# Kernel tuning notes

Measured on AMD Instinct MI355X. Metric: run time of the kernel, lower is better.

The kernel has to match this reference:

```python
import jax, jax.numpy as jnp
import numpy as np

N = 210          # sequence length (== module max_length cap)
DM = 2048        # input feature dim (major and minor)
DK = 1024        # key/query dim
DV = 1024        # value dim
K_CLIP = 32      # relative-position clipping distance


def _make_table(n, k):
    # table[i, j] = clip(j - i, -k, k) + k  (Shaw-style relative position index)
    rel = np.arange(n)[None, :] - np.arange(n)[:, None]
    return jnp.asarray(np.clip(rel, -k, k) + k, dtype=jnp.int32)


def setup_inputs() -> dict:
    key = jax.random.key(0)
    ks = jax.random.split(key, 7)
    X_major = jax.random.normal(ks[0], (N, DM), dtype=jnp.float32)
    X_minor = jax.random.normal(ks[1], (N, DM), dtype=jnp.float32)
    # Linear weights stored as [in, out] for x @ W
    s = 0.02
    Wq = jax.random.normal(ks[2], (DM, DK), dtype=jnp.float32) * s
    Wk = jax.random.normal(ks[3], (DM, DK), dtype=jnp.float32) * s
    Wv = jax.random.normal(ks[4], (DM, DV), dtype=jnp.float32) * s
    Wo = jax.random.normal(ks[5], (DV, DV), dtype=jnp.float32) * s
    wk = jax.random.normal(ks[6], (2 * K_CLIP + 1, DK), dtype=jnp.float32) * s
    table = _make_table(N, K_CLIP)
    return {"X_major": X_major, "X_minor": X_minor, "Wq": Wq, "Wk": Wk,
            "Wv": Wv, "Wo": Wo, "wk": wk, "table": table}


def reference(X_major, X_minor, Wq, Wk, Wv, Wo, wk, table):
    n = X_major.shape[0]
    scale = 1.0 / jnp.sqrt(jnp.asarray(Wq.shape[1], X_major.dtype))
    Q = X_major @ Wq                     # [n, dk]
    K = X_minor @ Wk                     # [n, dk]
    V = X_minor @ Wv                     # [n, dv]
    Qs = Q * scale
    S = Qs @ K.T                         # [n, n] content scores
    Rk = wk[table[:n, :n]]               # [n, n, dk] gathered rel-pos reps
    Sr = jnp.einsum('id,ijd->ij', Qs, Rk)  # [n, n] relative scores
    A = jax.nn.softmax(S + Sr, axis=-1)  # [n, n]
    Y = (A @ V) @ Wo                     # [n, dv]
    return (Y, A)
```

## Files before the change

kernel.cpp:

```cpp
#include <hip/hip_runtime.h>

typedef short bf16x8 __attribute__((ext_vector_type(8)));
typedef float f32x4 __attribute__((ext_vector_type(4)));

#define MFMA16(a, b, c) __builtin_amdgcn_mfma_f32_16x16x32_bf16(a, b, c, 0, 0, 0)

__device__ inline short f2bf(float f) {
  unsigned u = __builtin_bit_cast(unsigned, f);
  u += 0x7FFFu + ((u >> 16) & 1u);
  return (short)(u >> 16);
}
__device__ inline unsigned pack2(float lo, float hi) {
  unsigned a = __builtin_bit_cast(unsigned, lo) + 0x8000u;
  unsigned b = __builtin_bit_cast(unsigned, hi) + 0x8000u;
  return __builtin_amdgcn_perm(b, a, 0x07060302u);
}

__device__ inline void async_cp16(const void* g, void* l) {
  __builtin_amdgcn_global_load_lds(
      (const __attribute__((address_space(1))) unsigned int*)g,
      (__attribute__((address_space(3))) unsigned int*)l, 16, 0, 0);
}

#define SWZ(r, c) ((((r) << 4) + ((c) ^ ((r) & 7))) << 3)


__global__ __launch_bounds__(256) void k_prep(const float* __restrict__ xmaj,
                                              const float* __restrict__ xmin,
                                              const float* __restrict__ wkin,
                                              const float* __restrict__ Wq,
                                              const float* __restrict__ Wk,
                                              const float* __restrict__ Wv,
                                              const float* __restrict__ Wo,
                                              short* __restrict__ xmaj_bf,
                                              short* __restrict__ xmin_bf,
                                              short* __restrict__ kwb,
                                              short* __restrict__ wqt,
                                              short* __restrict__ wkt,
                                              short* __restrict__ wvt,
                                              short* __restrict__ wot) {
  __shared__ short tile[64][72];
  int b = blockIdx.x, t = threadIdx.x;
  if (b < 512) {
    int idx = b * 256 + t;
    if (idx < 107520) {
      float4 v = ((const float4*)xmaj)[idx];
      ((uint2*)xmaj_bf)[idx] = make_uint2(pack2(v.x, v.y), pack2(v.z, v.w));
      float4 u = ((const float4*)xmin)[idx];
      ((uint2*)xmin_bf)[idx] = make_uint2(pack2(u.x, u.y), pack2(u.z, u.w));
    }
    if (idx < 16640) {
      float4 v = ((const float4*)wkin)[idx];
      ((uint2*)(kwb + 210 * 1024))[idx] = make_uint2(pack2(v.x, v.y), pack2(v.z, v.w));
    }
    if (idx < 1664) ((uint4*)(kwb + 275 * 1024))[idx] = make_uint4(0, 0, 0, 0);
    return;
  }
  const float* W;
  short* Wt;
  int kt, nt, dstK;
  if (b < 2048) {
    int wi = (b - 512) >> 9, tl = (b - 512) & 511;
    W = wi == 0 ? Wq : (wi == 1 ? Wk : Wv);
    Wt = wi == 0 ? wqt : (wi == 1 ? wkt : wvt);
    kt = tl >> 4; nt = tl & 15; dstK = 2048;
  } else {
    int tl = b - 2048;
    W = Wo; Wt = wot; kt = tl >> 4; nt = tl & 15; dstK = 1024;
  }
  int k0 = kt * 64, n0 = nt * 64;
  int kp = t >> 4, nl4 = (t & 15) * 4;
  for (int h = 0; h < 2; ++h) {
    int kpp = kp + h * 16;
    const float* g = W + (size_t)(k0 + 2 * kpp) * 1024 + n0 + nl4;
    float4 u = *(const float4*)g;
    float4 v = *(const float4*)(g + 1024);
    *(unsigned*)&tile[nl4 + 0][2 * kpp] = pack2(u.x, v.x);
    *(unsigned*)&tile[nl4 + 1][2 * kpp] = pack2(u.y, v.y);
    *(unsigned*)&tile[nl4 + 2][2 * kpp] = pack2(u.z, v.z);
    *(unsigned*)&tile[nl4 + 3][2 * kpp] = pack2(u.w, v.w);
  }
  __syncthreads();
  int nl = t >> 2, cq = t & 3;
  for (int h = 0; h < 2; ++h) {
    int c = cq + h * 4;
    *(uint4*)(Wt + (size_t)(n0 + nl) * dstK + k0 + c * 8) = *(const uint4*)&tile[nl][c * 8];
  }
}

__global__ __launch_bounds__(256, 1) void k_qkv(const short* __restrict__ xmaj,
                                                const short* __restrict__ xmin,
                                                const short* __restrict__ wqt,
                                                const short* __restrict__ wkt,
                                                const short* __restrict__ wvt,
                                                short* __restrict__ qs,
                                                short* __restrict__ kwb,
                                                short* __restrict__ vt) {
  __shared__ short As[64 * 128];
  __shared__ short Bs[64 * 128];
  int b = blockIdx.x, t = threadIdx.x;
  int x = b & 7, s = b >> 3;
  int ntile = x * 6 + (s >> 2), mtile = s & 3;
  int nn0 = ntile * 64;
  int mat = nn0 >> 10, ncol0 = nn0 & 1023, m0 = mtile * 64;
  const short* A = (mat == 0) ? xmaj : xmin;
  const short* Bt = (mat == 0) ? wqt : (mat == 1 ? wkt : wvt);
  int lane = t & 63, w = t >> 6;
  int wm = w >> 1, wn = w & 1;
  int l15 = lane & 15, l4 = lane >> 4;
  f32x4 acc[2][2] = {};

  for (int k0 = 0; k0 < 2048; k0 += 128) {
    __syncthreads();
#pragma unroll
    for (int j = 0; j < 4; ++j) {
      int sj = t + j * 256;
      int r = sj >> 4, cg = (sj & 15) ^ (r & 7);
      async_cp16(A + (size_t)(m0 + r) * 2048 + k0 + cg * 8, &As[(w * 64 + j * 256) * 8]);
    }
#pragma unroll
    for (int j = 0; j < 4; ++j) {
      int sj = t + j * 256;
      int r = sj >> 4, cg = (sj & 15) ^ (r & 7);
      async_cp16(Bt + (size_t)(ncol0 + r) * 2048 + k0 + cg * 8, &Bs[(w * 64 + j * 256) * 8]);
    }
    __syncthreads();
#pragma unroll
    for (int kk = 0; kk < 4; ++kk) {
      int c = kk * 4 + l4;
      int ra0 = wm * 32 + l15, ra1 = ra0 + 16;
      int rb0 = wn * 32 + l15, rb1 = rb0 + 16;
      bf16x8 a0 = *(const bf16x8*)&As[SWZ(ra0, c)];
      bf16x8 a1 = *(const bf16x8*)&As[SWZ(ra1, c)];
      bf16x8 b0 = *(const bf16x8*)&Bs[SWZ(rb0, c)];
      bf16x8 b1 = *(const bf16x8*)&Bs[SWZ(rb1, c)];
      acc[0][0] = MFMA16(a0, b0, acc[0][0]);
      acc[0][1] = MFMA16(a0, b1, acc[0][1]);
      acc[1][0] = MFMA16(a1, b0, acc[1][0]);
      acc[1][1] = MFMA16(a1, b1, acc[1][1]);
    }
  }

  if (mat < 2) {
    float scale = (mat == 0) ? 0.03125f : 1.0f;
    short* dst = (mat == 0) ? qs : kwb;
#pragma unroll
    for (int mi = 0; mi < 2; ++mi)
#pragma unroll
      for (int ni = 0; ni < 2; ++ni) {
        int r0 = m0 + wm * 32 + mi * 16 + l4 * 4;
        int c = ncol0 + wn * 32 + ni * 16 + l15;
        for (int j = 0; j < 4; ++j) {
          int r = r0 + j;
          if (r < 210) dst[r * 1024 + c] = f2bf(acc[mi][ni][j] * scale);
        }
      }
  } else {
    __syncthreads();
#pragma unroll
    for (int mi = 0; mi < 2; ++mi)
#pragma unroll
      for (int ni = 0; ni < 2; ++ni) {
        int nl = wn * 32 + ni * 16 + l15;
        int ml0 = wm * 32 + mi * 16 + l4 * 4;
        for (int j = 0; j < 4; ++j) As[nl * 72 + ml0 + j] = f2bf(acc[mi][ni][j]);
      }
    __syncthreads();
    for (int h = 0; h < 2; ++h) {
      int idx = t + h * 256;
      int nl = idx >> 3, c8 = idx & 7;
      int mg0 = m0 + c8 * 8;
      short* dstp = vt + (ncol0 + nl) * 256 + mg0;
      if (mg0 + 8 <= 210) {
        *(uint4*)dstp = *(const uint4*)&As[nl * 72 + c8 * 8];
      } else {
        for (int e = 0; e < 8; ++e)
          if (mg0 + e < 210) dstp[e] = As[nl * 72 + c8 * 8 + e];
      }
    }
  }
}

__global__ __launch_bounds__(256, 1) void k_sprime(const short* __restrict__ qs,
                                                   const short* __restrict__ kwb,
                                                   float* __restrict__ Sp) {
  __shared__ short As[32 * 128];
  __shared__ short Bs[64 * 128];
  int n0 = blockIdx.x * 64, m0 = blockIdx.y * 32;
  int t = threadIdx.x, lane = t & 63, w = t >> 6;
  int l15 = lane & 15, l4 = lane >> 4;
  f32x4 acc[2] = {};

  for (int k0 = 0; k0 < 1024; k0 += 128) {
    __syncthreads();
#pragma unroll
    for (int j = 0; j < 2; ++j) {
      int sj = t + j * 256;
      int r = sj >> 4, cg = (sj & 15) ^ (r & 7);
      async_cp16(qs + (size_t)(m0 + r) * 1024 + k0 + cg * 8, &As[(w * 64 + j * 256) * 8]);
    }
#pragma unroll
    for (int j = 0; j < 4; ++j) {
      int sj = t + j * 256;
      int r = sj >> 4, cg = (sj & 15) ^ (r & 7);
      async_cp16(kwb + (size_t)(n0 + r) * 1024 + k0 + cg * 8, &Bs[(w * 64 + j * 256) * 8]);
    }
    __syncthreads();
#pragma unroll
    for (int kk = 0; kk < 4; ++kk) {
      int c = kk * 4 + l4;
      int rb = w * 16 + l15;
      bf16x8 a0 = *(const bf16x8*)&As[SWZ(l15, c)];
      bf16x8 a1 = *(const bf16x8*)&As[SWZ(16 + l15, c)];
      bf16x8 bb = *(const bf16x8*)&Bs[SWZ(rb, c)];
      acc[0] = MFMA16(a0, bb, acc[0]);
      acc[1] = MFMA16(a1, bb, acc[1]);
    }
  }
#pragma unroll
  for (int mi = 0; mi < 2; ++mi) {
    int r0 = m0 + mi * 16 + l4 * 4;
    int col = n0 + w * 16 + l15;
    for (int j = 0; j < 4; ++j) Sp[(r0 + j) * 320 + col] = acc[mi][j];
  }
}

__global__ __launch_bounds__(256) void k_softmax(const float* __restrict__ Sp,
                                                 const int* __restrict__ table,
                                                 short* __restrict__ Abf,
                                                 float* __restrict__ outA) {
  int i = blockIdx.x, t = threadIdx.x;
  if (i >= 210) {
    Abf[i * 256 + t] = 0;
    return;
  }
  __shared__ float srow[288];
  __shared__ float red[4];
  for (int j = t; j < 288; j += 256) srow[j] = Sp[i * 320 + j];
  __syncthreads();
  float logit = -1e30f;
  if (t < 210) {
    int tb = table[i * 210 + t];
    logit = srow[t] + srow[210 + tb];
  }
  float m = logit;
  for (int o = 32; o; o >>= 1) m = fmaxf(m, __shfl_xor(m, o));
  if ((t & 63) == 0) red[t >> 6] = m;
  __syncthreads();
  m = fmaxf(fmaxf(red[0], red[1]), fmaxf(red[2], red[3]));
  float e = (t < 210) ? __expf(logit - m) : 0.0f;
  float s = e;
  for (int o = 32; o; o >>= 1) s += __shfl_xor(s, o);
  __syncthreads();
  if ((t & 63) == 0) red[t >> 6] = s;
  __syncthreads();
  s = red[0] + red[1] + red[2] + red[3];
  float a = e / s;
  Abf[i * 256 + t] = (t < 210) ? f2bf(a) : (short)0;
  if (t < 210) outA[i * 210 + t] = a;
}

__global__ __launch_bounds__(256, 1) void k_av(const short* __restrict__ Abf,
                                               const short* __restrict__ vt,
                                               short* __restrict__ av) {
  __shared__ short As[64 * 128];
  __shared__ short Bs[64 * 128];
  int n0 = blockIdx.x * 64, m0 = blockIdx.y * 64;
  int t = threadIdx.x, lane = t & 63, w = t >> 6;
  int wm = w >> 1, wn = w & 1;
  int l15 = lane & 15, l4 = lane >> 4;
  f32x4 acc[2][2] = {};

  for (int k0 = 0; k0 < 256; k0 += 128) {
    __syncthreads();
#pragma unroll
    for (int j = 0; j < 4; ++j) {
      int sj = t + j * 256;
      int r = sj >> 4, cg = (sj & 15) ^ (r & 7);
      async_cp16(Abf + (size_t)(m0 + r) * 256 + k0 + cg * 8, &As[(w * 64 + j * 256) * 8]);
      async_cp16(vt + (size_t)(n0 + r) * 256 + k0 + cg * 8, &Bs[(w * 64 + j * 256) * 8]);
    }
    __syncthreads();
#pragma unroll
    for (int kk = 0; kk < 4; ++kk) {
      int c = kk * 4 + l4;
      int ra0 = wm * 32 + l15, ra1 = ra0 + 16;
      int rb0 = wn * 32 + l15, rb1 = rb0 + 16;
      bf16x8 a0 = *(const bf16x8*)&As[SWZ(ra0, c)];
      bf16x8 a1 = *(const bf16x8*)&As[SWZ(ra1, c)];
      bf16x8 b0 = *(const bf16x8*)&Bs[SWZ(rb0, c)];
      bf16x8 b1 = *(const bf16x8*)&Bs[SWZ(rb1, c)];
      acc[0][0] = MFMA16(a0, b0, acc[0][0]);
      acc[0][1] = MFMA16(a0, b1, acc[0][1]);
      acc[1][0] = MFMA16(a1, b0, acc[1][0]);
      acc[1][1] = MFMA16(a1, b1, acc[1][1]);
    }
  }
#pragma unroll
  for (int mi = 0; mi < 2; ++mi)
#pragma unroll
    for (int ni = 0; ni < 2; ++ni) {
      int r0 = m0 + wm * 32 + mi * 16 + l4 * 4;
      int c = n0 + wn * 32 + ni * 16 + l15;
      for (int j = 0; j < 4; ++j) {
        int r = r0 + j;
        if (r < 210) av[r * 1024 + c] = f2bf(acc[mi][ni][j]);
      }
    }
}

__global__ __launch_bounds__(256, 1) void k_y(const short* __restrict__ av,
                                              const short* __restrict__ wot,
                                              float* __restrict__ outY) {
  __shared__ short As[64 * 128];
  __shared__ short Bs[64 * 128];
  int n0 = blockIdx.x * 64, m0 = blockIdx.y * 64;
  int t = threadIdx.x, lane = t & 63, w = t >> 6;
  int wm = w >> 1, wn = w & 1;
  int l15 = lane & 15, l4 = lane >> 4;
  f32x4 acc[2][2] = {};

  for (int k0 = 0; k0 < 1024; k0 += 128) {
    __syncthreads();
#pragma unroll
    for (int j = 0; j < 4; ++j) {
      int sj = t + j * 256;
      int r = sj >> 4, cg = (sj & 15) ^ (r & 7);
      async_cp16(av + (size_t)(m0 + r) * 1024 + k0 + cg * 8, &As[(w * 64 + j * 256) * 8]);
      async_cp16(wot + (size_t)(n0 + r) * 1024 + k0 + cg * 8, &Bs[(w * 64 + j * 256) * 8]);
    }
    __syncthreads();
#pragma unroll
    for (int kk = 0; kk < 4; ++kk) {
      int c = kk * 4 + l4;
      int ra0 = wm * 32 + l15, ra1 = ra0 + 16;
      int rb0 = wn * 32 + l15, rb1 = rb0 + 16;
      bf16x8 a0 = *(const bf16x8*)&As[SWZ(ra0, c)];
      bf16x8 a1 = *(const bf16x8*)&As[SWZ(ra1, c)];
      bf16x8 b0 = *(const bf16x8*)&Bs[SWZ(rb0, c)];
      bf16x8 b1 = *(const bf16x8*)&Bs[SWZ(rb1, c)];
      acc[0][0] = MFMA16(a0, b0, acc[0][0]);
      acc[0][1] = MFMA16(a0, b1, acc[0][1]);
      acc[1][0] = MFMA16(a1, b0, acc[1][0]);
      acc[1][1] = MFMA16(a1, b1, acc[1][1]);
    }
  }
#pragma unroll
  for (int mi = 0; mi < 2; ++mi)
#pragma unroll
    for (int ni = 0; ni < 2; ++ni) {
      int r0 = m0 + wm * 32 + mi * 16 + l4 * 4;
      int c = n0 + wn * 32 + ni * 16 + l15;
      for (int j = 0; j < 4; ++j) {
        int r = r0 + j;
        if (r < 210) outY[r * 1024 + c] = acc[mi][ni][j];
      }
    }
}

extern "C" void kernel_launch(void* const* d_in, const int* in_sizes, int n_in,
                              void* d_out, int out_size, void* d_ws, size_t ws_size,
                              hipStream_t stream) {
  const float* Xmaj = (const float*)d_in[0];
  const float* Xmin = (const float*)d_in[1];
  const float* Wq = (const float*)d_in[2];
  const float* Wk = (const float*)d_in[3];
  const float* Wv = (const float*)d_in[4];
  const float* Wo = (const float*)d_in[5];
  const float* wk = (const float*)d_in[6];
  const int* table = (const int*)d_in[7];

  char* ws = (char*)d_ws;
  short* xmaj_bf = (short*)(ws + 0);
  short* xmin_bf = (short*)(ws + 1048576);
  short* qs = (short*)(ws + 2097152);
  short* kwb = (short*)(ws + 2621440);
  short* vt = (short*)(ws + 3276800);
  short* Abf = (short*)(ws + 3801088);
  short* av = (short*)(ws + 3932160);
  float* Sp = (float*)(ws + 4456448);
  short* wqt = (short*)(ws + 4743168);
  short* wkt = (short*)(ws + 8937472);
  short* wvt = (short*)(ws + 13131776);
  short* wot = (short*)(ws + 17326080);

  float* outY = (float*)d_out;
  float* outA = (float*)d_out + 215040;

  k_prep<<<2304, 256, 0, stream>>>(Xmaj, Xmin, wk, Wq, Wk, Wv, Wo,
                                   xmaj_bf, xmin_bf, kwb, wqt, wkt, wvt, wot);
  k_qkv<<<192, 256, 0, stream>>>(xmaj_bf, xmin_bf, wqt, wkt, wvt, qs, kwb, vt);
  k_sprime<<<dim3(5, 7), 256, 0, stream>>>(qs, kwb, Sp);
  k_softmax<<<256, 256, 0, stream>>>(Sp, table, Abf, outA);
  k_av<<<dim3(16, 4), 256, 0, stream>>>(Abf, vt, av);
  k_y<<<dim3(16, 4), 256, 0, stream>>>(av, wot, outY);
}
```

Measured before the change: 127.0 us.

## Reassociate output projection as A@(V@Wo) and fuse with score GEMM

Computes VW = V@Wo ahead of the softmax, inside a combined kernel that also runs the Q·K' score GEMM as independent blocks, with double-buffered async LDS loads. The final kernel then does a single A@VW GEMM with K=256 loaded in one shot. This drops one kernel launch and the serial av→Y dependency, and lets the V@Wo GEMM overlap the score computation. In exchange it adds an extra bf16 rounding of V@Wo, a different rounding order, and larger shared-memory buffers.

```diff
diff --git a/kernel.cpp b/kernel.cpp
--- a/kernel.cpp
+++ b/kernel.cpp
@@ -15,14 +15,15 @@
   unsigned b = __builtin_bit_cast(unsigned, hi) + 0x8000u;
   return __builtin_amdgcn_perm(b, a, 0x07060302u);
 }
-
 __device__ inline void async_cp16(const void* g, void* l) {
   __builtin_amdgcn_global_load_lds(
       (const __attribute__((address_space(1))) unsigned int*)g,
       (__attribute__((address_space(3))) unsigned int*)l, 16, 0, 0);
 }
-
 #define SWZ(r, c) ((((r) << 4) + ((c) ^ ((r) & 7))) << 3)
+__device__ inline int swz5(int r, int c) {
+  return ((r << 5) + ((c & ~7) | ((c ^ r) & 7))) << 3;
+}
 
 
 __global__ __launch_bounds__(256) void k_prep(const float* __restrict__ xmaj,
@@ -95,7 +96,7 @@
                                                 const short* __restrict__ wvt,
                                                 short* __restrict__ qs,
                                                 short* __restrict__ kwb,
-                                                short* __restrict__ vt) {
+                                                short* __restrict__ v) {
   __shared__ short As[64 * 128];
   __shared__ short Bs[64 * 128];
   int b = blockIdx.x, t = threadIdx.x;
@@ -141,87 +142,132 @@
     }
   }
 
-  if (mat < 2) {
-    float scale = (mat == 0) ? 0.03125f : 1.0f;
-    short* dst = (mat == 0) ? qs : kwb;
-#pragma unroll
-    for (int mi = 0; mi < 2; ++mi)
-#pragma unroll
-      for (int ni = 0; ni < 2; ++ni) {
-        int r0 = m0 + wm * 32 + mi * 16 + l4 * 4;
-        int c = ncol0 + wn * 32 + ni * 16 + l15;
-        for (int j = 0; j < 4; ++j) {
-          int r = r0 + j;
-          if (r < 210) dst[r * 1024 + c] = f2bf(acc[mi][ni][j] * scale);
-        }
-      }
+  float scale = (mat == 0) ? 0.03125f : 1.0f;
+  short* dst = (mat == 0) ? qs : (mat == 1 ? kwb : v);
+#pragma unroll
+  for (int mi = 0; mi < 2; ++mi)
+#pragma unroll
+    for (int ni = 0; ni < 2; ++ni) {
+      int r0 = m0 + wm * 32 + mi * 16 + l4 * 4;
+      int c = ncol0 + wn * 32 + ni * 16 + l15;
+      for (int j = 0; j < 4; ++j) {
+        int r = r0 + j;
+        if (r < 210) dst[r * 1024 + c] = f2bf(acc[mi][ni][j] * scale);
+      }
+    }
+}
+
+__global__ __launch_bounds__(256, 1) void k_mid(const short* __restrict__ qs,
+                                                const short* __restrict__ kwb,
+                                                const short* __restrict__ v,
+                                                const short* __restrict__ wot,
+                                                float* __restrict__ Sp,
+                                                short* __restrict__ vwt) {
+  __shared__ short As[2][64 * 128];
+  __shared__ short Bs[2][64 * 128];
+  int b = blockIdx.x, t = threadIdx.x;
+  int lane = t & 63, w = t >> 6;
+  int l15 = lane & 15, l4 = lane >> 4;
+
+  if (b < 35) {
+    int n0 = (b % 5) * 64, m0 = (b / 5) * 32;
+    f32x4 acc[2] = {};
+    auto issue = [&](int p) {
+      int k0 = p * 128, d = p & 1;
+#pragma unroll
+      for (int j = 0; j < 2; ++j) {
+        int sj = t + j * 256;
+        int r = sj >> 4, cg = (sj & 15) ^ (r & 7);
+        async_cp16(qs + (size_t)(m0 + r) * 1024 + k0 + cg * 8, &As[d][(j * 256 + w * 64) * 8]);
+      }
+#pragma unroll
+      for (int j = 0; j < 4; ++j) {
+        int sj = t + j * 256;
+        int r = sj >> 4, cg = (sj & 15) ^ (r & 7);
+        async_cp16(kwb + (size_t)(n0 + r) * 1024 + k0 + cg * 8, &Bs[d][(j * 256 + w * 64) * 8]);
+      }
+    };
+    issue(0);
+#pragma unroll 1
+    for (int p = 0; p < 8; ++p) {
+      __syncthreads();
+      if (p < 7) issue(p + 1);
+      int d = p & 1;
+#pragma unroll
+      for (int kk = 0; kk < 4; ++kk) {
+        int c = kk * 4 + l4;
+        bf16x8 a0 = *(const bf16x8*)&As[d][SWZ(l15, c)];
+        bf16x8 a1 = *(const bf16x8*)&As[d][SWZ(16 + l15, c)];
+        bf16x8 bb = *(const bf16x8*)&Bs[d][SWZ(w * 16 + l15, c)];
+        acc[0] = MFMA16(a0, bb, acc[0]);
+        acc[1] = MFMA16(a1, bb, acc[1]);
+      }
+    }
+#pragma unroll
+    for (int mi = 0; mi < 2; ++mi) {
+      int r0 = m0 + mi * 16 + l4 * 4;
+      int col = n0 + w * 16 + l15;
+      for (int j = 0; j < 4; ++j) Sp[(r0 + j) * 320 + col] = acc[mi][j];
+    }
   } else {
+    int bb = b - 35;
+    int n0 = (bb & 15) * 64, m0 = (bb >> 4) * 64;
+    int wm = w >> 1, wn = w & 1;
+    f32x4 acc[2][2] = {};
+    auto issue = [&](int p) {
+      int k0 = p * 128, d = p & 1;
+#pragma unroll
+      for (int j = 0; j < 4; ++j) {
+        int sj = t + j * 256;
+        int r = sj >> 4, cg = (sj & 15) ^ (r & 7);
+        async_cp16(v + (size_t)(m0 + r) * 1024 + k0 + cg * 8, &As[d][(j * 256 + w * 64) * 8]);
+        async_cp16(wot + (size_t)(n0 + r) * 1024 + k0 + cg * 8, &Bs[d][(j * 256 + w * 64) * 8]);
+      }
+    };
+    issue(0);
+#pragma unroll 1
+    for (int p = 0; p < 8; ++p) {
+      __syncthreads();
+      if (p < 7) issue(p + 1);
+      int d = p & 1;
+#pragma unroll
+      for (int kk = 0; kk < 4; ++kk) {
+        int c = kk * 4 + l4;
+        int ra0 = wm * 32 + l15, ra1 = ra0 + 16;
+        int rb0 = wn * 32 + l15, rb1 = rb0 + 16;
+        bf16x8 a0 = *(const bf16x8*)&As[d][SWZ(ra0, c)];
+        bf16x8 a1 = *(const bf16x8*)&As[d][SWZ(ra1, c)];
+        bf16x8 b0 = *(const bf16x8*)&Bs[d][SWZ(rb0, c)];
+        bf16x8 b1 = *(const bf16x8*)&Bs[d][SWZ(rb1, c)];
+        acc[0][0] = MFMA16(a0, b0, acc[0][0]);
+        acc[0][1] = MFMA16(a0, b1, acc[0][1]);
+        acc[1][0] = MFMA16(a1, b0, acc[1][0]);
+        acc[1][1] = MFMA16(a1, b1, acc[1][1]);
+      }
+    }
     __syncthreads();
+    short* scr = &As[0][0];
 #pragma unroll
     for (int mi = 0; mi < 2; ++mi)
 #pragma unroll
       for (int ni = 0; ni < 2; ++ni) {
         int nl = wn * 32 + ni * 16 + l15;
         int ml0 = wm * 32 + mi * 16 + l4 * 4;
-        for (int j = 0; j < 4; ++j) As[nl * 72 + ml0 + j] = f2bf(acc[mi][ni][j]);
+        for (int j = 0; j < 4; ++j) scr[nl * 72 + ml0 + j] = f2bf(acc[mi][ni][j]);
       }
     __syncthreads();
     for (int h = 0; h < 2; ++h) {
       int idx = t + h * 256;
       int nl = idx >> 3, c8 = idx & 7;
       int mg0 = m0 + c8 * 8;
-      short* dstp = vt + (ncol0 + nl) * 256 + mg0;
+      short* dstp = vwt + (size_t)(n0 + nl) * 256 + mg0;
       if (mg0 + 8 <= 210) {
-        *(uint4*)dstp = *(const uint4*)&As[nl * 72 + c8 * 8];
+        *(uint4*)dstp = *(const uint4*)&scr[nl * 72 + c8 * 8];
       } else {
         for (int e = 0; e < 8; ++e)
-          if (mg0 + e < 210) dstp[e] = As[nl * 72 + c8 * 8 + e];
-      }
-    }
-  }
-}
-
-__global__ __launch_bounds__(256, 1) void k_sprime(const short* __restrict__ qs,
-                                                   const short* __restrict__ kwb,
-                                                   float* __restrict__ Sp) {
-  __shared__ short As[32 * 128];
-  __shared__ short Bs[64 * 128];
-  int n0 = blockIdx.x * 64, m0 = blockIdx.y * 32;
-  int t = threadIdx.x, lane = t & 63, w = t >> 6;
-  int l15 = lane & 15, l4 = lane >> 4;
-  f32x4 acc[2] = {};
-
-  for (int k0 = 0; k0 < 1024; k0 += 128) {
-    __syncthreads();
-#pragma unroll
-    for (int j = 0; j < 2; ++j) {
-      int sj = t + j * 256;
-      int r = sj >> 4, cg = (sj & 15) ^ (r & 7);
-      async_cp16(qs + (size_t)(m0 + r) * 1024 + k0 + cg * 8, &As[(w * 64 + j * 256) * 8]);
-    }
-#pragma unroll
-    for (int j = 0; j < 4; ++j) {
-      int sj = t + j * 256;
-      int r = sj >> 4, cg = (sj & 15) ^ (r & 7);
-      async_cp16(kwb + (size_t)(n0 + r) * 1024 + k0 + cg * 8, &Bs[(w * 64 + j * 256) * 8]);
-    }
-    __syncthreads();
-#pragma unroll
-    for (int kk = 0; kk < 4; ++kk) {
-      int c = kk * 4 + l4;
-      int rb = w * 16 + l15;
-      bf16x8 a0 = *(const bf16x8*)&As[SWZ(l15, c)];
-      bf16x8 a1 = *(const bf16x8*)&As[SWZ(16 + l15, c)];
-      bf16x8 bb = *(const bf16x8*)&Bs[SWZ(rb, c)];
-      acc[0] = MFMA16(a0, bb, acc[0]);
-      acc[1] = MFMA16(a1, bb, acc[1]);
-    }
-  }
-#pragma unroll
-  for (int mi = 0; mi < 2; ++mi) {
-    int r0 = m0 + mi * 16 + l4 * 4;
-    int col = n0 + w * 16 + l15;
-    for (int j = 0; j < 4; ++j) Sp[(r0 + j) * 320 + col] = acc[mi][j];
+          if (mg0 + e < 210) dstp[e] = scr[nl * 72 + c8 * 8 + e];
+      }
+    }
   }
 }
 
@@ -260,90 +306,40 @@
   if (t < 210) outA[i * 210 + t] = a;
 }
 
-__global__ __launch_bounds__(256, 1) void k_av(const short* __restrict__ Abf,
-                                               const short* __restrict__ vt,
-                                               short* __restrict__ av) {
-  __shared__ short As[64 * 128];
-  __shared__ short Bs[64 * 128];
+__global__ __launch_bounds__(256, 1) void k_fin(const short* __restrict__ Abf,
+                                                const short* __restrict__ vwt,
+                                                float* __restrict__ outY) {
+  __shared__ short As[64 * 256];
+  __shared__ short Bs[64 * 256];
   int n0 = blockIdx.x * 64, m0 = blockIdx.y * 64;
   int t = threadIdx.x, lane = t & 63, w = t >> 6;
   int wm = w >> 1, wn = w & 1;
   int l15 = lane & 15, l4 = lane >> 4;
+
+#pragma unroll
+  for (int j = 0; j < 8; ++j) {
+    int sj = t + j * 256;
+    int r = sj >> 5, c = sj & 31;
+    int cg = (c & ~7) | ((c ^ r) & 7);
+    async_cp16(Abf + (size_t)(m0 + r) * 256 + cg * 8, &As[(j * 256 + w * 64) * 8]);
+    async_cp16(vwt + (size_t)(n0 + r) * 256 + cg * 8, &Bs[(j * 256 + w * 64) * 8]);
+  }
+  __syncthreads();
+
   f32x4 acc[2][2] = {};
-
-  for (int k0 = 0; k0 < 256; k0 += 128) {
-    __syncthreads();
-#pragma unroll
-    for (int j = 0; j < 4; ++j) {
-      int sj = t + j * 256;
-      int r = sj >> 4, cg = (sj & 15) ^ (r & 7);
-      async_cp16(Abf + (size_t)(m0 + r) * 256 + k0 + cg * 8, &As[(w * 64 + j * 256) * 8]);
-      async_cp16(vt + (size_t)(n0 + r) * 256 + k0 + cg * 8, &Bs[(w * 64 + j * 256) * 8]);
-    }
-    __syncthreads();
-#pragma unroll
-    for (int kk = 0; kk < 4; ++kk) {
-      int c = kk * 4 + l4;
-      int ra0 = wm * 32 + l15, ra1 = ra0 + 16;
-      int rb0 = wn * 32 + l15, rb1 = rb0 + 16;
-      bf16x8 a0 = *(const bf16x8*)&As[SWZ(ra0, c)];
-      bf16x8 a1 = *(const bf16x8*)&As[SWZ(ra1, c)];
-      bf16x8 b0 = *(const bf16x8*)&Bs[SWZ(rb0, c)];
-      bf16x8 b1 = *(const bf16x8*)&Bs[SWZ(rb1, c)];
-      acc[0][0] = MFMA16(a0, b0, acc[0][0]);
-      acc[0][1] = MFMA16(a0, b1, acc[0][1]);
-      acc[1][0] = MFMA16(a1, b0, acc[1][0]);
-      acc[1][1] = MFMA16(a1, b1, acc[1][1]);
-    }
-  }
-#pragma unroll
-  for (int mi = 0; mi < 2; ++mi)
-#pragma unroll
-    for (int ni = 0; ni < 2; ++ni) {
-      int r0 = m0 + wm * 32 + mi * 16 + l4 * 4;
-      int c = n0 + wn * 32 + ni * 16 + l15;
-      for (int j = 0; j < 4; ++j) {
-        int r = r0 + j;
-        if (r < 210) av[r * 1024 + c] = f2bf(acc[mi][ni][j]);
-      }
-    }
-}
-
-__global__ __launch_bounds__(256, 1) void k_y(const short* __restrict__ av,
-                                              const short* __restrict__ wot,
-                                              float* __restrict__ outY) {
-  __shared__ short As[64 * 128];
-  __shared__ short Bs[64 * 128];
-  int n0 = blockIdx.x * 64, m0 = blockIdx.y * 64;
-  int t = threadIdx.x, lane = t & 63, w = t >> 6;
-  int wm = w >> 1, wn = w & 1;
-  int l15 = lane & 15, l4 = lane >> 4;
-  f32x4 acc[2][2] = {};
-
-  for (int k0 = 0; k0 < 1024; k0 += 128) {
-    __syncthreads();
-#pragma unroll
-    for (int j = 0; j < 4; ++j) {
-      int sj = t + j * 256;
-      int r = sj >> 4, cg = (sj & 15) ^ (r & 7);
-      async_cp16(av + (size_t)(m0 + r) * 1024 + k0 + cg * 8, &As[(w * 64 + j * 256) * 8]);
-      async_cp16(wot + (size_t)(n0 + r) * 1024 + k0 + cg * 8, &Bs[(w * 64 + j * 256) * 8]);
-    }
-    __syncthreads();
-#pragma unroll
-    for (int kk = 0; kk < 4; ++kk) {
-      int c = kk * 4 + l4;
-      int ra0 = wm * 32 + l15, ra1 = ra0 + 16;
-      int rb0 = wn * 32 + l15, rb1 = rb0 + 16;
-      bf16x8 a0 = *(const bf16x8*)&As[SWZ(ra0, c)];
-      bf16x8 a1 = *(const bf16x8*)&As[SWZ(ra1, c)];
-      bf16x8 b0 = *(const bf16x8*)&Bs[SWZ(rb0, c)];
-      bf16x8 b1 = *(const bf16x8*)&Bs[SWZ(rb1, c)];
-      acc[0][0] = MFMA16(a0, b0, acc[0][0]);
-      acc[0][1] = MFMA16(a0, b1, acc[0][1]);
-      acc[1][0] = MFMA16(a1, b0, acc[1][0]);
-      acc[1][1] = MFMA16(a1, b1, acc[1][1]);
-    }
+#pragma unroll
+  for (int kk = 0; kk < 8; ++kk) {
+    int c = kk * 4 + l4;
+    int ra0 = wm * 32 + l15, ra1 = ra0 + 16;
+    int rb0 = wn * 32 + l15, rb1 = rb0 + 16;
+    bf16x8 a0 = *(const bf16x8*)&As[swz5(ra0, c)];
+    bf16x8 a1 = *(const bf16x8*)&As[swz5(ra1, c)];
+    bf16x8 b0 = *(const bf16x8*)&Bs[swz5(rb0, c)];
+    bf16x8 b1 = *(const bf16x8*)&Bs[swz5(rb1, c)];
+    acc[0][0] = MFMA16(a0, b0, acc[0][0]);
+    acc[0][1] = MFMA16(a0, b1, acc[0][1]);
+    acc[1][0] = MFMA16(a1, b0, acc[1][0]);
+    acc[1][1] = MFMA16(a1, b1, acc[1][1]);
   }
 #pragma unroll
   for (int mi = 0; mi < 2; ++mi)
@@ -375,9 +371,9 @@
   short* xmin_bf = (short*)(ws + 1048576);
   short* qs = (short*)(ws + 2097152);
   short* kwb = (short*)(ws + 2621440);
-  short* vt = (short*)(ws + 3276800);
+  short* vwt = (short*)(ws + 3276800);
   short* Abf = (short*)(ws + 3801088);
-  short* av = (short*)(ws + 3932160);
+  short* v = (short*)(ws + 3932160);
   float* Sp = (float*)(ws + 4456448);
   short* wqt = (short*)(ws + 4743168);
   short* wkt = (short*)(ws + 8937472);
@@ -389,9 +385,8 @@
 
   k_prep<<<2304, 256, 0, stream>>>(Xmaj, Xmin, wk, Wq, Wk, Wv, Wo,
                                    xmaj_bf, xmin_bf, kwb, wqt, wkt, wvt, wot);
-  k_qkv<<<192, 256, 0, stream>>>(xmaj_bf, xmin_bf, wqt, wkt, wvt, qs, kwb, vt);
-  k_sprime<<<dim3(5, 7), 256, 0, stream>>>(qs, kwb, Sp);
+  k_qkv<<<192, 256, 0, stream>>>(xmaj_bf, xmin_bf, wqt, wkt, wvt, qs, kwb, v);
+  k_mid<<<99, 256, 0, stream>>>(qs, kwb, v, wot, Sp, vwt);
   k_softmax<<<256, 256, 0, stream>>>(Sp, table, Abf, outA);
-  k_av<<<dim3(16, 4), 256, 0, stream>>>(Abf, vt, av);
-  k_y<<<dim3(16, 4), 256, 0, stream>>>(av, wot, outY);
-}
+  k_fin<<<dim3(16, 4), 256, 0, stream>>>(Abf, vwt, outY);
+}
```

Result: faster. 120.8 us (-4.9%).
